# Optimization experiments

Measured on AMD Instinct MI355X. Metric: run time of the kernel, lower is better.

Reference implementation:

```python
import jax, jax.numpy as jnp
import numpy as np
import math

D_MODEL = 512
N_HEADS = 8
D_K = D_MODEL // N_HEADS
N_SAMPLES = 16
BETA = 1.0
SCALE = 1.0 / math.sqrt(D_K)
PROPOSAL_TEMP = 0.5


def setup_inputs() -> dict:
    key = jax.random.key(0)
    ks = jax.random.split(key, 9)
    B, S = 2, 512
    x = jax.random.normal(ks[0], (B, S, D_MODEL), dtype=jnp.float32)
    init = lambda k: jax.random.normal(k, (D_MODEL, D_MODEL), dtype=jnp.float32) * 0.02
    return {
        "x": x,
        "Wq": init(ks[1]), "bq": jnp.zeros((D_MODEL,), jnp.float32),
        "Wk": init(ks[2]), "bk": jnp.zeros((D_MODEL,), jnp.float32),
        "Wv": init(ks[3]), "bv": jnp.zeros((D_MODEL,), jnp.float32),
        "Wo": init(ks[4]), "bo": jnp.zeros((D_MODEL,), jnp.float32),
    }


def _importance_sampled_weights(scores):
    # scores: [B,H,S,S]. Replicates the per-row Python loop, fully vectorized.
    B, H, Sq, Sk = scores.shape
    target = jax.nn.softmax(scores * BETA, axis=-1)            # [B,H,Sq,Sk]
    # optimal proposal: 0.5*target + 0.5*uniform
    prop = PROPOSAL_TEMP * target + (1.0 - PROPOSAL_TEMP) / Sk
    R = B * H * Sq
    tf = target.reshape(R, Sk)
    pf = prop.reshape(R, Sk)
    # tsu_backend.sample_binary_layer(log(p/(1-p))) == Bernoulli(p) sampling
    s = jax.random.bernoulli(jax.random.key(42), pf[:, None, :], (R, N_SAMPLES, Sk))
    # importance weight = prod(target[sel]) / (prod(prop[sel]) * prod(1-prop[~sel]))
    pt = jnp.prod(jnp.where(s, tf[:, None, :], 1.0), axis=-1)                 # [R,N]
    pp = jnp.prod(jnp.where(s, pf[:, None, :], 1.0 - pf[:, None, :]), axis=-1)
    valid = (s.sum(-1) > 0) & (pp > 0)
    w = jnp.where(valid, pt / jnp.maximum(pp, 1e-38), 0.0)
    ws = w.sum(-1, keepdims=True)
    w = jnp.where(ws > 0, w / jnp.maximum(ws, 1e-38), 1.0 / N_SAMPLES)        # [R,N]
    wa = jnp.einsum('rn,rnk->rk', w, s.astype(jnp.float32))                   # [R,Sk]
    was = wa.sum(-1, keepdims=True)
    wa = jnp.where(was > 0, wa / jnp.maximum(was, 1e-38), 1.0 / Sk)
    return wa.reshape(B, H, Sq, Sk)


def reference(x, Wq, bq, Wk, bk, Wv, bv, Wo, bo):
    B, S, Dm = x.shape
    proj = lambda W, b: (x @ W + b).reshape(B, S, N_HEADS, D_K).transpose(0, 2, 1, 3)
    Q = proj(Wq, bq)  # [B,H,S,dk]
    K = proj(Wk, bk)
    V = proj(Wv, bv)
    scores = jnp.einsum('bhqd,bhkd->bhqk', Q, K) * SCALE
    # torch builds weights via torch.tensor(...) which detaches => constant w.r.t. params
    attn = jax.lax.stop_gradient(_importance_sampled_weights(scores))
    out = jnp.einsum('bhqk,bhkd->bhqd', attn, V)
    out = out.transpose(0, 2, 1, 3).reshape(B, S, Dm)
    return out @ Wo + bo
```

## Files before the change

kernel.cpp:

```cpp
#include <hip/hip_runtime.h>
#include <cstdint>
#include <cstddef>


#define ROTL(x, r) __builtin_rotateleft32((x), (r))

#define QR8(s)                                                                \
  x0[0]+=x1[0];x0[1]+=x1[1];x0[2]+=x1[2];x0[3]+=x1[3];                        \
  x0[4]+=x1[4];x0[5]+=x1[5];x0[6]+=x1[6];x0[7]+=x1[7];                        \
  x1[0]=ROTL(x1[0],s);x1[1]=ROTL(x1[1],s);x1[2]=ROTL(x1[2],s);                \
  x1[3]=ROTL(x1[3],s);x1[4]=ROTL(x1[4],s);x1[5]=ROTL(x1[5],s);                \
  x1[6]=ROTL(x1[6],s);x1[7]=ROTL(x1[7],s);                                    \
  x1[0]^=x0[0];x1[1]^=x0[1];x1[2]^=x0[2];x1[3]^=x0[3];                        \
  x1[4]^=x0[4];x1[5]^=x0[5];x1[6]^=x0[6];x1[7]^=x0[7];
#define INJ8(X, Y)                                                            \
  x0[0]+=(X);x0[1]+=(X);x0[2]+=(X);x0[3]+=(X);                                \
  x0[4]+=(X);x0[5]+=(X);x0[6]+=(X);x0[7]+=(X);                                \
  x1[0]+=(Y);x1[1]+=(Y);x1[2]+=(Y);x1[3]+=(Y);                                \
  x1[4]+=(Y);x1[5]+=(Y);x1[6]+=(Y);x1[7]+=(Y);
#define INJ8Y(Y)                                                              \
  x1[0]+=(Y);x1[1]+=(Y);x1[2]+=(Y);x1[3]+=(Y);                                \
  x1[4]+=(Y);x1[5]+=(Y);x1[6]+=(Y);x1[7]+=(Y);

__global__ __launch_bounds__(256)
void qkv_gemm(const float* __restrict__ x,
              const float* __restrict__ Wq, const float* __restrict__ bq,
              const float* __restrict__ Wk, const float* __restrict__ bk,
              const float* __restrict__ Wv, const float* __restrict__ bv,
              float* __restrict__ Qw, float* __restrict__ KTw,
              float* __restrict__ Vw) {
  const float* W; const float* bias; float* out;
  if (blockIdx.z == 0)      { W = Wq; bias = bq; out = Qw; }
  else if (blockIdx.z == 1) { W = Wk; bias = bk; out = KTw; }
  else                      { W = Wv; bias = bv; out = Vw; }

  __shared__ float At[32][68];
  __shared__ float Bs[32][64];
  __shared__ __align__(16) float T2[64][68];
  const int tid = threadIdx.x;
  const int tx = tid & 15, ty = tid >> 4;
  const int row0 = blockIdx.x * 64, col0 = blockIdx.y * 64;
  float acc[4][4] = {};

  for (int kk = 0; kk < 512; kk += 32) {
    const int ar = tid >> 2;
#pragma unroll
    for (int i = 0; i < 2; ++i) {
      const int kc = ((tid & 3) << 3) + (i << 2);
      const float4 a4 =
          *(const float4*)&x[(size_t)(row0 + ar) * 512 + kk + kc];
      At[kc + 0][ar] = a4.x; At[kc + 1][ar] = a4.y;
      At[kc + 2][ar] = a4.z; At[kc + 3][ar] = a4.w;
    }
#pragma unroll
    for (int i = 0; i < 2; ++i) {
      const int idx = tid + (i << 8);
      const int br = idx >> 4, bc = (idx & 15) << 2;
      *(float4*)&Bs[br][bc] =
          *(const float4*)&W[(size_t)(kk + br) * 512 + col0 + bc];
    }
    __syncthreads();
#pragma unroll
    for (int p = 0; p < 32; ++p) {
      const float4 a4 = *(const float4*)&At[p][ty << 2];
      const float4 b4 = *(const float4*)&Bs[p][tx << 2];
      acc[0][0] = fmaf(a4.x, b4.x, acc[0][0]); acc[0][1] = fmaf(a4.x, b4.y, acc[0][1]);
      acc[0][2] = fmaf(a4.x, b4.z, acc[0][2]); acc[0][3] = fmaf(a4.x, b4.w, acc[0][3]);
      acc[1][0] = fmaf(a4.y, b4.x, acc[1][0]); acc[1][1] = fmaf(a4.y, b4.y, acc[1][1]);
      acc[1][2] = fmaf(a4.y, b4.z, acc[1][2]); acc[1][3] = fmaf(a4.y, b4.w, acc[1][3]);
      acc[2][0] = fmaf(a4.z, b4.x, acc[2][0]); acc[2][1] = fmaf(a4.z, b4.y, acc[2][1]);
      acc[2][2] = fmaf(a4.z, b4.z, acc[2][2]); acc[2][3] = fmaf(a4.z, b4.w, acc[2][3]);
      acc[3][0] = fmaf(a4.w, b4.x, acc[3][0]); acc[3][1] = fmaf(a4.w, b4.y, acc[3][1]);
      acc[3][2] = fmaf(a4.w, b4.z, acc[3][2]); acc[3][3] = fmaf(a4.w, b4.w, acc[3][3]);
    }
    __syncthreads();
  }
  if (blockIdx.z == 1) {
#pragma unroll
    for (int i = 0; i < 4; ++i) {
#pragma unroll
      for (int j = 0; j < 4; ++j) {
        const int col = col0 + (tx << 2) + j;
        T2[(tx << 2) + j][(ty << 2) + i] = acc[i][j] + bias[col];
      }
    }
    __syncthreads();
    const int c = tid >> 2, seg = tid & 3;
    const int b = row0 >> 9, h = col0 >> 6;
    const int s0 = (row0 & 511) + (seg << 4);
    float* dst = KTw + (((size_t)(b * 8 + h) * 64 + c) << 9) + s0;
#pragma unroll
    for (int i2 = 0; i2 < 4; ++i2) {
      const float4 v4 = *(const float4*)&T2[c][(seg << 4) + (i2 << 2)];
      *(float4*)&dst[i2 << 2] = v4;
    }
  } else {
#pragma unroll
    for (int i = 0; i < 4; ++i) {
      const int row = row0 + (ty << 2) + i;
      const int b = row >> 9, s = row & 511;
#pragma unroll
      for (int j = 0; j < 4; ++j) {
        const int col = col0 + (tx << 2) + j;
        const int h = col >> 6, d = col & 63;
        out[(((size_t)(b * 8 + h) * 512 + s) * 64) + d] = acc[i][j] + bias[col];
      }
    }
  }
}

__global__ __launch_bounds__(256)
void out_gemm(const float* __restrict__ A, const float* __restrict__ W,
              const float* __restrict__ bias, float* __restrict__ C) {
  __shared__ float At[32][68];
  __shared__ float Bs[32][64];
  const int tid = threadIdx.x;
  const int tx = tid & 15, ty = tid >> 4;
  const int row0 = blockIdx.x * 64, col0 = blockIdx.y * 64;
  float acc[4][4] = {};

  for (int kk = 0; kk < 512; kk += 32) {
    const int ar = tid >> 2;
#pragma unroll
    for (int i = 0; i < 2; ++i) {
      const int kc = ((tid & 3) << 3) + (i << 2);
      const float4 a4 =
          *(const float4*)&A[(size_t)(row0 + ar) * 512 + kk + kc];
      At[kc + 0][ar] = a4.x; At[kc + 1][ar] = a4.y;
      At[kc + 2][ar] = a4.z; At[kc + 3][ar] = a4.w;
    }
#pragma unroll
    for (int i = 0; i < 2; ++i) {
      const int idx = tid + (i << 8);
      const int br = idx >> 4, bc = (idx & 15) << 2;
      *(float4*)&Bs[br][bc] =
          *(const float4*)&W[(size_t)(kk + br) * 512 + col0 + bc];
    }
    __syncthreads();
#pragma unroll
    for (int p = 0; p < 32; ++p) {
      const float4 a4 = *(const float4*)&At[p][ty << 2];
      const float4 b4 = *(const float4*)&Bs[p][tx << 2];
      acc[0][0] = fmaf(a4.x, b4.x, acc[0][0]); acc[0][1] = fmaf(a4.x, b4.y, acc[0][1]);
      acc[0][2] = fmaf(a4.x, b4.z, acc[0][2]); acc[0][3] = fmaf(a4.x, b4.w, acc[0][3]);
      acc[1][0] = fmaf(a4.y, b4.x, acc[1][0]); acc[1][1] = fmaf(a4.y, b4.y, acc[1][1]);
      acc[1][2] = fmaf(a4.y, b4.z, acc[1][2]); acc[1][3] = fmaf(a4.y, b4.w, acc[1][3]);
      acc[2][0] = fmaf(a4.z, b4.x, acc[2][0]); acc[2][1] = fmaf(a4.z, b4.y, acc[2][1]);
      acc[2][2] = fmaf(a4.z, b4.z, acc[2][2]); acc[2][3] = fmaf(a4.z, b4.w, acc[2][3]);
      acc[3][0] = fmaf(a4.w, b4.x, acc[3][0]); acc[3][1] = fmaf(a4.w, b4.y, acc[3][1]);
      acc[3][2] = fmaf(a4.w, b4.z, acc[3][2]); acc[3][3] = fmaf(a4.w, b4.w, acc[3][3]);
    }
    __syncthreads();
  }
#pragma unroll
  for (int i = 0; i < 4; ++i) {
    const int row = row0 + (ty << 2) + i;
#pragma unroll
    for (int j = 0; j < 4; ++j) {
      const int col = col0 + (tx << 2) + j;
      C[(size_t)row * 512 + col] = acc[i][j] + bias[col];
    }
  }
}

__global__ __launch_bounds__(256)
void scores_softmax(const float* __restrict__ Q, const float* __restrict__ KT,
                    float* __restrict__ tf_g) {
  const int blk = blockIdx.x;
  const int bh = blk >> 7, q0 = (blk & 127) << 2;
  const int tid = threadIdx.x;
  __shared__ __align__(16) float qs[4][64];
  __shared__ float redm[4][4], reds[4][4];
  qs[tid >> 6][tid & 63] =
      Q[((size_t)bh * 512 + q0 + (tid >> 6)) * 64 + (tid & 63)];
  __syncthreads();

  float sc[4][2];
#pragma unroll
  for (int ii = 0; ii < 2; ++ii) {
    const int k = tid + ii * 256;
    const float* Kp = KT + (size_t)bh * 64 * 512 + k;
    float a0 = 0.f, a1 = 0.f, a2 = 0.f, a3 = 0.f;
#pragma unroll
    for (int d4 = 0; d4 < 16; ++d4) {
      const float4 v0 = ((const float4*)qs[0])[d4];
      const float4 v1 = ((const float4*)qs[1])[d4];
      const float4 v2 = ((const float4*)qs[2])[d4];
      const float4 v3 = ((const float4*)qs[3])[d4];
      const float k0 = Kp[(size_t)(d4 * 4 + 0) * 512];
      const float k1 = Kp[(size_t)(d4 * 4 + 1) * 512];
      const float k2 = Kp[(size_t)(d4 * 4 + 2) * 512];
      const float k3 = Kp[(size_t)(d4 * 4 + 3) * 512];
      a0 = fmaf(v0.x, k0, a0); a0 = fmaf(v0.y, k1, a0);
      a0 = fmaf(v0.z, k2, a0); a0 = fmaf(v0.w, k3, a0);
      a1 = fmaf(v1.x, k0, a1); a1 = fmaf(v1.y, k1, a1);
      a1 = fmaf(v1.z, k2, a1); a1 = fmaf(v1.w, k3, a1);
      a2 = fmaf(v2.x, k0, a2); a2 = fmaf(v2.y, k1, a2);
      a2 = fmaf(v2.z, k2, a2); a2 = fmaf(v2.w, k3, a2);
      a3 = fmaf(v3.x, k0, a3); a3 = fmaf(v3.y, k1, a3);
      a3 = fmaf(v3.z, k2, a3); a3 = fmaf(v3.w, k3, a3);
    }
    sc[0][ii] = a0 * 0.125f; sc[1][ii] = a1 * 0.125f;
    sc[2][ii] = a2 * 0.125f; sc[3][ii] = a3 * 0.125f;
  }
  float mx[4];
#pragma unroll
  for (int i = 0; i < 4; ++i) mx[i] = fmaxf(sc[i][0], sc[i][1]);
  for (int m = 1; m < 64; m <<= 1) {
#pragma unroll
    for (int i = 0; i < 4; ++i) mx[i] = fmaxf(mx[i], __shfl_xor(mx[i], m));
  }
  if ((tid & 63) == 0) {
    const int w = tid >> 6;
#pragma unroll
    for (int i = 0; i < 4; ++i) redm[i][w] = mx[i];
  }
  __syncthreads();
  float ex[4][2], sm[4];
#pragma unroll
  for (int i = 0; i < 4; ++i) {
    const float rm = fmaxf(fmaxf(redm[i][0], redm[i][1]),
                           fmaxf(redm[i][2], redm[i][3]));
    ex[i][0] = expf(sc[i][0] - rm);
    ex[i][1] = expf(sc[i][1] - rm);
    sm[i] = ex[i][0] + ex[i][1];
  }
  for (int m = 1; m < 64; m <<= 1) {
#pragma unroll
    for (int i = 0; i < 4; ++i) sm[i] += __shfl_xor(sm[i], m);
  }
  if ((tid & 63) == 0) {
    const int w = tid >> 6;
#pragma unroll
    for (int i = 0; i < 4; ++i) reds[i][w] = sm[i];
  }
  __syncthreads();
#pragma unroll
  for (int i = 0; i < 4; ++i) {
    const float tot = reds[i][0] + reds[i][1] + reds[i][2] + reds[i][3];
    tf_g[((size_t)bh * 512 + q0 + i) * 512 + tid]       = ex[i][0] / tot;
    tf_g[((size_t)bh * 512 + q0 + i) * 512 + tid + 256] = ex[i][1] / tot;
  }
}

__global__ __launch_bounds__(256)
void sample_attnv(const float* __restrict__ tf_g, const float* __restrict__ V,
                  float* __restrict__ ao) {
  const int r = blockIdx.x;
  const int b = r >> 12, h = (r >> 9) & 7, q = r & 511;
  const int tid = threadIdx.x;
  __shared__ float tf[512];
  __shared__ __align__(16) uint32_t pscu2[512];
  __shared__ float wa[512];
  __shared__ float wr[16];
  __shared__ float redc[8];
  __shared__ float psum[4][64];
  __shared__ int   list[512];
  __shared__ int   cnt;

  if (tid == 0) cnt = 0;
  {
    const float t0 = tf_g[(size_t)r * 512 + tid];
    const float t1 = tf_g[(size_t)r * 512 + tid + 256];
    tf[tid] = t0; tf[tid + 256] = t1;
    wa[tid] = 0.f; wa[tid + 256] = 0.f;
    const float p0 = fmaf(0.5f, t0, 0.0009765625f);
    const float p1 = fmaf(0.5f, t1, 0.0009765625f);
    {
      const int k = tid;
      pscu2[(((k & 31) >> 2) << 6) + ((k >> 5) << 2) + (k & 3)] =
          ((uint32_t)ceilf(p0 * 8388608.0f)) << 9;
    }
    {
      const int k = tid + 256;
      pscu2[(((k & 31) >> 2) << 6) + ((k >> 5) << 2) + (k & 3)] =
          ((uint32_t)ceilf(p1 * 8388608.0f)) << 9;
    }
    float ql = (1.f - p0) * (1.f - p1);
    for (int m = 1; m < 64; m <<= 1) ql *= __shfl_xor(ql, m);
    if ((tid & 63) == 0) redc[4 + (tid >> 6)] = ql;
  }
  __syncthreads();
  const float Qrow = redc[4] * redc[5] * redc[6] * redc[7];

  const int n = tid >> 4, t = tid & 15;
  const int k0 = t << 5;
  const uint32_t cbase =
      (uint32_t)r * 8192u + (uint32_t)n * 512u + (uint32_t)k0 + 42u;
  uint32_t bits = 0u;
#pragma unroll
  for (int jb = 0; jb < 32; jb += 8) {
    uint32_t x0[8], x1[8];
#pragma unroll
    for (int i = 0; i < 8; ++i) {
      const uint32_t c = cbase + (uint32_t)(jb + i);
      x0[i] = c;
      x1[i] = ROTL(c, 13) ^ c;
    }
    QR8(15) QR8(26) QR8(6)
    INJ8(42u, 0x1BD11BF1u)
    QR8(17) QR8(29) QR8(16) QR8(24)
    INJ8(0x1BD11BF0u, 2u)
    QR8(13) QR8(15) QR8(26) QR8(6)
    INJ8Y(45u)
    QR8(17) QR8(29) QR8(16) QR8(24)
    INJ8(42u, 0x1BD11BF4u)
    QR8(13) QR8(15) QR8(26) QR8(6)
    INJ8(0x1BD11BF0u, 5u)
    const uint4 pA = *(const uint4*)&pscu2[((jb >> 2) << 6) + (t << 2)];
    const uint4 pB = *(const uint4*)&pscu2[(((jb >> 2) + 1) << 6) + (t << 2)];
    bits |= (uint32_t)((x0[0] ^ x1[0]) < pA.x) << (jb + 0);
    bits |= (uint32_t)((x0[1] ^ x1[1]) < pA.y) << (jb + 1);
    bits |= (uint32_t)((x0[2] ^ x1[2]) < pA.z) << (jb + 2);
    bits |= (uint32_t)((x0[3] ^ x1[3]) < pA.w) << (jb + 3);
    bits |= (uint32_t)((x0[4] ^ x1[4]) < pB.x) << (jb + 4);
    bits |= (uint32_t)((x0[5] ^ x1[5]) < pB.y) << (jb + 5);
    bits |= (uint32_t)((x0[6] ^ x1[6]) < pB.z) << (jb + 6);
    bits |= (uint32_t)((x0[7] ^ x1[7]) < pB.w) << (jb + 7);
  }

  float ptl = 1.f, ratl = 1.f;
  int cl = __popc(bits);
  {
    uint32_t bb = bits;
    while (bb) {
      const int j = __builtin_ctz(bb);
      bb &= bb - 1u;
      const float tv = tf[k0 + j];
      const float p = fmaf(0.5f, tv, 0.0009765625f);
      ptl *= tv;
      ratl *= p / (1.f - p);
    }
  }
#pragma unroll
  for (int m = 1; m < 16; m <<= 1) {
    ptl *= __shfl_xor(ptl, m);
    ratl *= __shfl_xor(ratl, m);
    cl += __shfl_xor(cl, m);
  }
  if (t == 0) {
    const float pp = Qrow * ratl;
    wr[n] = (cl > 0 && pp > 0.f) ? (ptl / fmaxf(pp, 1e-38f)) : 0.f;
  }
  __syncthreads();
  float wsum = 0.f;
#pragma unroll
  for (int m2 = 0; m2 < 16; ++m2) wsum += wr[m2];
  const float wn = (wsum > 0.f) ? (wr[n] / fmaxf(wsum, 1e-38f)) : 0.0625f;
  {
    uint32_t bb = bits;
    while (bb) {
      const int j = __builtin_ctz(bb);
      bb &= bb - 1u;
      atomicAdd(&wa[k0 + j], wn);
    }
  }
  __syncthreads();

  float sp = wa[tid] + wa[tid + 256];
  for (int m = 1; m < 64; m <<= 1) sp += __shfl_xor(sp, m);
  if ((tid & 63) == 0) redc[tid >> 6] = sp;
  if (wa[tid] > 0.f)       { const int i = atomicAdd(&cnt, 1); list[i] = tid; }
  if (wa[tid + 256] > 0.f) { const int i = atomicAdd(&cnt, 1); list[i] = tid + 256; }
  __syncthreads();
  const float was = redc[0] + redc[1] + redc[2] + redc[3];
  const int nnz = cnt;

  const int g = tid >> 6, d = tid & 63;
  const float* Vb = V + ((size_t)(b * 8 + h) * 512) * 64;
  float acc = 0.f;
  if (was > 0.f) {
    const float inv = 1.f / fmaxf(was, 1e-38f);
    for (int i = g; i < nnz; i += 4) {
      const int k = list[i];
      acc = fmaf(wa[k] * inv, Vb[(size_t)k * 64 + d], acc);
    }
  } else {
    for (int k = g; k < 512; k += 4) acc += Vb[(size_t)k * 64 + d];
    acc *= 0.001953125f;
  }
  psum[g][d] = acc;
  __syncthreads();
  if (g == 0) {
    ao[((size_t)(b * 512 + q) * 512) + h * 64 + d] =
        psum[0][d] + psum[1][d] + psum[2][d] + psum[3][d];
  }
}

extern "C" void kernel_launch(void* const* d_in, const int* in_sizes, int n_in,
                              void* d_out, int out_size, void* d_ws,
                              size_t ws_size, hipStream_t stream) {
  const float* x  = (const float*)d_in[0];
  const float* Wq = (const float*)d_in[1];
  const float* bq = (const float*)d_in[2];
  const float* Wk = (const float*)d_in[3];
  const float* bk = (const float*)d_in[4];
  const float* Wv = (const float*)d_in[5];
  const float* bv = (const float*)d_in[6];
  const float* Wo = (const float*)d_in[7];
  const float* bo = (const float*)d_in[8];
  float* out = (float*)d_out;

  float* ws = (float*)d_ws;
  float* Qw = ws;
  float* KT = ws + 524288;
  float* Vw = ws + 1048576;
  float* tf = ws + 1572864;
  float* ao = ws + 5767168;

  dim3 gq(16, 8, 3);
  qkv_gemm<<<gq, 256, 0, stream>>>(x, Wq, bq, Wk, bk, Wv, bv, Qw, KT, Vw);
  scores_softmax<<<2048, 256, 0, stream>>>(Qw, KT, tf);
  sample_attnv<<<8192, 256, 0, stream>>>(tf, Vw, ao);
  dim3 go(16, 8);
  out_gemm<<<go, 256, 0, stream>>>(ao, Wo, bo, out);
}
```

Baseline: 276.9 us.

## Fuse scores/softmax into sampling kernel, drop global target-probability buffer

Merges the QK^T score and softmax kernel into the per-row sampling kernel, so each block computes its own row of target probabilities directly into shared memory. This removes the 16 MB round-trip of the tf buffer through global memory and one kernel launch. In exchange each block handles only one query row, so K is reloaded per row rather than shared across four rows, which raises L2 traffic. The K-transpose store in the QKV GEMM is also simplified to direct strided scalar writes in place of the shared-memory staged float4 transpose, which may make those stores less coalesced.

New measurement: 260.8 us. 5.8% less time.

```diff
diff --git a/kernel.cpp b/kernel.cpp
--- a/kernel.cpp
+++ b/kernel.cpp
@@ -36,7 +36,6 @@
 
   __shared__ float At[32][68];
   __shared__ float Bs[32][64];
-  __shared__ __align__(16) float T2[64][68];
   const int tid = threadIdx.x;
   const int tx = tid & 15, ty = tid >> 4;
   const int row0 = blockIdx.x * 64, col0 = blockIdx.y * 64;
@@ -75,36 +74,20 @@
     }
     __syncthreads();
   }
-  if (blockIdx.z == 1) {
-#pragma unroll
-    for (int i = 0; i < 4; ++i) {
-#pragma unroll
-      for (int j = 0; j < 4; ++j) {
-        const int col = col0 + (tx << 2) + j;
-        T2[(tx << 2) + j][(ty << 2) + i] = acc[i][j] + bias[col];
-      }
-    }
-    __syncthreads();
-    const int c = tid >> 2, seg = tid & 3;
-    const int b = row0 >> 9, h = col0 >> 6;
-    const int s0 = (row0 & 511) + (seg << 4);
-    float* dst = KTw + (((size_t)(b * 8 + h) * 64 + c) << 9) + s0;
-#pragma unroll
-    for (int i2 = 0; i2 < 4; ++i2) {
-      const float4 v4 = *(const float4*)&T2[c][(seg << 4) + (i2 << 2)];
-      *(float4*)&dst[i2 << 2] = v4;
-    }
-  } else {
-#pragma unroll
-    for (int i = 0; i < 4; ++i) {
-      const int row = row0 + (ty << 2) + i;
-      const int b = row >> 9, s = row & 511;
-#pragma unroll
-      for (int j = 0; j < 4; ++j) {
-        const int col = col0 + (tx << 2) + j;
-        const int h = col >> 6, d = col & 63;
-        out[(((size_t)(b * 8 + h) * 512 + s) * 64) + d] = acc[i][j] + bias[col];
-      }
+  const bool isK = (blockIdx.z == 1);
+#pragma unroll
+  for (int i = 0; i < 4; ++i) {
+    const int row = row0 + (ty << 2) + i;
+    const int b = row >> 9, s = row & 511;
+#pragma unroll
+    for (int j = 0; j < 4; ++j) {
+      const int col = col0 + (tx << 2) + j;
+      const int h = col >> 6, d = col & 63;
+      const float v = acc[i][j] + bias[col];
+      if (isK)
+        out[(((size_t)(b * 8 + h) * 64 + d) * 512) + s] = v;
+      else
+        out[(((size_t)(b * 8 + h) * 512 + s) * 64) + d] = v;
     }
   }
 }
@@ -164,91 +147,14 @@
 }
 
 __global__ __launch_bounds__(256)
-void scores_softmax(const float* __restrict__ Q, const float* __restrict__ KT,
-                    float* __restrict__ tf_g) {
-  const int blk = blockIdx.x;
-  const int bh = blk >> 7, q0 = (blk & 127) << 2;
+void fused_sample(const float* __restrict__ Q, const float* __restrict__ KT,
+                  const float* __restrict__ V, float* __restrict__ ao) {
+  const int r = blockIdx.x;
+  const int bh = r >> 9, q = r & 511;
+  const int b = r >> 12, h = (r >> 9) & 7;
   const int tid = threadIdx.x;
-  __shared__ __align__(16) float qs[4][64];
-  __shared__ float redm[4][4], reds[4][4];
-  qs[tid >> 6][tid & 63] =
-      Q[((size_t)bh * 512 + q0 + (tid >> 6)) * 64 + (tid & 63)];
-  __syncthreads();
-
-  float sc[4][2];
-#pragma unroll
-  for (int ii = 0; ii < 2; ++ii) {
-    const int k = tid + ii * 256;
-    const float* Kp = KT + (size_t)bh * 64 * 512 + k;
-    float a0 = 0.f, a1 = 0.f, a2 = 0.f, a3 = 0.f;
-#pragma unroll
-    for (int d4 = 0; d4 < 16; ++d4) {
-      const float4 v0 = ((const float4*)qs[0])[d4];
-      const float4 v1 = ((const float4*)qs[1])[d4];
-      const float4 v2 = ((const float4*)qs[2])[d4];
-      const float4 v3 = ((const float4*)qs[3])[d4];
-      const float k0 = Kp[(size_t)(d4 * 4 + 0) * 512];
-      const float k1 = Kp[(size_t)(d4 * 4 + 1) * 512];
-      const float k2 = Kp[(size_t)(d4 * 4 + 2) * 512];
-      const float k3 = Kp[(size_t)(d4 * 4 + 3) * 512];
-      a0 = fmaf(v0.x, k0, a0); a0 = fmaf(v0.y, k1, a0);
-      a0 = fmaf(v0.z, k2, a0); a0 = fmaf(v0.w, k3, a0);
-      a1 = fmaf(v1.x, k0, a1); a1 = fmaf(v1.y, k1, a1);
-      a1 = fmaf(v1.z, k2, a1); a1 = fmaf(v1.w, k3, a1);
-      a2 = fmaf(v2.x, k0, a2); a2 = fmaf(v2.y, k1, a2);
-      a2 = fmaf(v2.z, k2, a2); a2 = fmaf(v2.w, k3, a2);
-      a3 = fmaf(v3.x, k0, a3); a3 = fmaf(v3.y, k1, a3);
-      a3 = fmaf(v3.z, k2, a3); a3 = fmaf(v3.w, k3, a3);
-    }
-    sc[0][ii] = a0 * 0.125f; sc[1][ii] = a1 * 0.125f;
-    sc[2][ii] = a2 * 0.125f; sc[3][ii] = a3 * 0.125f;
-  }
-  float mx[4];
-#pragma unroll
-  for (int i = 0; i < 4; ++i) mx[i] = fmaxf(sc[i][0], sc[i][1]);
-  for (int m = 1; m < 64; m <<= 1) {
-#pragma unroll
-    for (int i = 0; i < 4; ++i) mx[i] = fmaxf(mx[i], __shfl_xor(mx[i], m));
-  }
-  if ((tid & 63) == 0) {
-    const int w = tid >> 6;
-#pragma unroll
-    for (int i = 0; i < 4; ++i) redm[i][w] = mx[i];
-  }
-  __syncthreads();
-  float ex[4][2], sm[4];
-#pragma unroll
-  for (int i = 0; i < 4; ++i) {
-    const float rm = fmaxf(fmaxf(redm[i][0], redm[i][1]),
-                           fmaxf(redm[i][2], redm[i][3]));
-    ex[i][0] = expf(sc[i][0] - rm);
-    ex[i][1] = expf(sc[i][1] - rm);
-    sm[i] = ex[i][0] + ex[i][1];
-  }
-  for (int m = 1; m < 64; m <<= 1) {
-#pragma unroll
-    for (int i = 0; i < 4; ++i) sm[i] += __shfl_xor(sm[i], m);
-  }
-  if ((tid & 63) == 0) {
-    const int w = tid >> 6;
-#pragma unroll
-    for (int i = 0; i < 4; ++i) reds[i][w] = sm[i];
-  }
-  __syncthreads();
-#pragma unroll
-  for (int i = 0; i < 4; ++i) {
-    const float tot = reds[i][0] + reds[i][1] + reds[i][2] + reds[i][3];
-    tf_g[((size_t)bh * 512 + q0 + i) * 512 + tid]       = ex[i][0] / tot;
-    tf_g[((size_t)bh * 512 + q0 + i) * 512 + tid + 256] = ex[i][1] / tot;
-  }
-}
-
-__global__ __launch_bounds__(256)
-void sample_attnv(const float* __restrict__ tf_g, const float* __restrict__ V,
-                  float* __restrict__ ao) {
-  const int r = blockIdx.x;
-  const int b = r >> 12, h = (r >> 9) & 7, q = r & 511;
-  const int tid = threadIdx.x;
+  __shared__ __align__(16) float qs[64];
+  __shared__ float red[8];
   __shared__ float tf[512];
   __shared__ __align__(16) uint32_t pscu2[512];
   __shared__ float wa[512];
@@ -259,11 +165,43 @@
   __shared__ int   cnt;
 
   if (tid == 0) cnt = 0;
+  if (tid < 64) qs[tid] = Q[((size_t)bh * 512 + q) * 64 + tid];
+  __syncthreads();
+
+  float sc[2];
+#pragma unroll
+  for (int ii = 0; ii < 2; ++ii) {
+    const int k = tid + (ii << 8);
+    const float* Kp = KT + (size_t)bh * 64 * 512 + k;
+    float s = 0.f;
+#pragma unroll
+    for (int d4 = 0; d4 < 16; ++d4) {
+      const float4 qv = ((const float4*)qs)[d4];
+      const float k0 = Kp[(size_t)(d4 * 4 + 0) * 512];
+      const float k1 = Kp[(size_t)(d4 * 4 + 1) * 512];
+      const float k2 = Kp[(size_t)(d4 * 4 + 2) * 512];
+      const float k3 = Kp[(size_t)(d4 * 4 + 3) * 512];
+      s = fmaf(qv.x, k0, s); s = fmaf(qv.y, k1, s);
+      s = fmaf(qv.z, k2, s); s = fmaf(qv.w, k3, s);
+    }
+    sc[ii] = s * 0.125f;
+  }
+  float mx = fmaxf(sc[0], sc[1]);
+  for (int m = 1; m < 64; m <<= 1) mx = fmaxf(mx, __shfl_xor(mx, m));
+  if ((tid & 63) == 0) red[tid >> 6] = mx;
+  __syncthreads();
+  const float rowmax = fmaxf(fmaxf(red[0], red[1]), fmaxf(red[2], red[3]));
+  const float e0 = expf(sc[0] - rowmax);
+  const float e1 = expf(sc[1] - rowmax);
+  float ssum = e0 + e1;
+  for (int m = 1; m < 64; m <<= 1) ssum += __shfl_xor(ssum, m);
+  if ((tid & 63) == 0) red[4 + (tid >> 6)] = ssum;
+  __syncthreads();
+  const float tot = red[4] + red[5] + red[6] + red[7];
+  const float t0 = e0 / tot, t1 = e1 / tot;
+  tf[tid] = t0; tf[tid + 256] = t1;
+  wa[tid] = 0.f; wa[tid + 256] = 0.f;
   {
-    const float t0 = tf_g[(size_t)r * 512 + tid];
-    const float t1 = tf_g[(size_t)r * 512 + tid + 256];
-    tf[tid] = t0; tf[tid + 256] = t1;
-    wa[tid] = 0.f; wa[tid + 256] = 0.f;
     const float p0 = fmaf(0.5f, t0, 0.0009765625f);
     const float p1 = fmaf(0.5f, t1, 0.0009765625f);
     {
@@ -284,9 +222,9 @@
   const float Qrow = redc[4] * redc[5] * redc[6] * redc[7];
 
   const int n = tid >> 4, t = tid & 15;
-  const int k0 = t << 5;
+  const int k0i = t << 5;
   const uint32_t cbase =
-      (uint32_t)r * 8192u + (uint32_t)n * 512u + (uint32_t)k0 + 42u;
+      (uint32_t)r * 8192u + (uint32_t)n * 512u + (uint32_t)k0i + 42u;
   uint32_t bits = 0u;
 #pragma unroll
   for (int jb = 0; jb < 32; jb += 8) {
@@ -326,7 +264,7 @@
     while (bb) {
       const int j = __builtin_ctz(bb);
       bb &= bb - 1u;
-      const float tv = tf[k0 + j];
+      const float tv = tf[k0i + j];
       const float p = fmaf(0.5f, tv, 0.0009765625f);
       ptl *= tv;
       ratl *= p / (1.f - p);
@@ -352,7 +290,7 @@
     while (bb) {
       const int j = __builtin_ctz(bb);
       bb &= bb - 1u;
-      atomicAdd(&wa[k0 + j], wn);
+      atomicAdd(&wa[k0i + j], wn);
     }
   }
   __syncthreads();
@@ -405,13 +343,11 @@
   float* Qw = ws;
   float* KT = ws + 524288;
   float* Vw = ws + 1048576;
-  float* tf = ws + 1572864;
-  float* ao = ws + 5767168;
+  float* ao = ws + 1572864;
 
   dim3 gq(16, 8, 3);
   qkv_gemm<<<gq, 256, 0, stream>>>(x, Wq, bq, Wk, bk, Wv, bv, Qw, KT, Vw);
-  scores_softmax<<<2048, 256, 0, stream>>>(Qw, KT, tf);
-  sample_attnv<<<8192, 256, 0, stream>>>(tf, Vw, ao);
+  fused_sample<<<8192, 256, 0, stream>>>(Qw, KT, Vw, ao);
   dim3 go(16, 8);
   out_gemm<<<go, 256, 0, stream>>>(ao, Wo, bo, out);
 }
```
